# Performance work log

Measured on AMD Instinct MI355X. Metric: run time of the kernel, lower is better.

## Reference

```python
import jax, jax.numpy as jnp
import numpy as np

B, C_IN, C_OUT, H, W = 64, 1024, 1024, 16, 16
HEADS, C_RED = 8, 512  # reduced_ch = 1024 // 2
N = H * W
EPS = 1e-5  # BatchNorm eps (eval mode, running stats)
NEG_SLOPE = 0.2  # PyG GATConv default leaky_relu slope


def build_grid_edge_index(P, Pw):
    # 4-neighbor grid + one self-loop per node, directed [2, E]
    edges = []
    for i in range(P):
        for j in range(Pw):
            u = i * Pw + j
            if i - 1 >= 0: edges.append([u, u - Pw])
            if i + 1 < P:  edges.append([u, u + Pw])
            if j - 1 >= 0: edges.append([u, u - 1])
            if j + 1 < Pw: edges.append([u, u + 1])
            edges.append([u, u])
    return jnp.asarray(np.array(edges, dtype=np.int32).T)


def setup_inputs() -> dict:
    key = jax.random.key(0)
    ks = jax.random.split(key, 10)
    x = jax.random.normal(ks[0], (B, C_IN, H, W), jnp.float32)
    w_reduce = jax.random.normal(ks[1], (C_RED, C_IN), jnp.float32) * 0.02
    g_red = jnp.ones((C_RED,), jnp.float32); b_red = jnp.zeros((C_RED,), jnp.float32)
    m_red = jax.random.normal(ks[2], (C_RED,), jnp.float32) * 0.1
    v_red = jax.random.uniform(ks[3], (C_RED,), jnp.float32) + 0.5
    w_gat = jax.random.normal(ks[4], (C_RED, HEADS * C_RED), jnp.float32) * 0.02
    att_src = jax.random.normal(ks[5], (HEADS, C_RED), jnp.float32) * 0.1
    att_dst = jax.random.normal(ks[6], (HEADS, C_RED), jnp.float32) * 0.1
    gat_bias = jnp.zeros((C_RED,), jnp.float32)
    w_restore = jax.random.normal(ks[7], (C_OUT, C_RED), jnp.float32) * 0.02
    g_res = jnp.ones((C_OUT,), jnp.float32); b_res = jnp.zeros((C_OUT,), jnp.float32)
    m_res = jax.random.normal(ks[8], (C_OUT,), jnp.float32) * 0.1
    v_res = jax.random.uniform(ks[9], (C_OUT,), jnp.float32) + 0.5
    edge_index = build_grid_edge_index(H, W)
    return dict(x=x, w_reduce=w_reduce, g_red=g_red, b_red=b_red, m_red=m_red, v_red=v_red,
                w_gat=w_gat, att_src=att_src, att_dst=att_dst, gat_bias=gat_bias,
                w_restore=w_restore, g_res=g_res, b_res=b_res, m_res=m_res, v_res=v_res,
                edge_index=edge_index)


def _bn(x, g, b, m, v):  # channel-last, eval mode
    return (x - m) * (g * jax.lax.rsqrt(v + EPS)) + b


def reference(x, w_reduce, g_red, b_red, m_red, v_red, w_gat, att_src, att_dst,
              gat_bias, w_restore, g_res, b_res, m_res, v_res, edge_index):
    xh = jnp.transpose(x, (0, 2, 3, 1))                 # [B,H,W,C_in] NHWC
    res = xh                                            # identity residual (C_in == C_out)
    xr = jax.nn.relu(_bn(xh @ w_reduce.T, g_red, b_red, m_red, v_red))  # [B,H,W,C_red]
    nodes = xr.reshape(B, N, C_RED)                     # per-sample grid graph nodes

    # --- GATConv (heads=HEADS, concat=False), batched over B ---
    xp = (nodes @ w_gat).reshape(B, N, HEADS, C_RED)    # projected per-head features
    a_src = jnp.einsum('bnhc,hc->bnh', xp, att_src)
    a_dst = jnp.einsum('bnhc,hc->bnh', xp, att_dst)
    src, dst = edge_index[0], edge_index[1]
    logits = jax.nn.leaky_relu(a_src[:, src] + a_dst[:, dst], NEG_SLOPE)  # [B,E,HEADS]
    seg_max = jax.vmap(lambda a: jax.ops.segment_max(a, dst, num_segments=N))(logits)
    e = jnp.exp(logits - seg_max[:, dst])
    seg_sum = jax.vmap(lambda a: jax.ops.segment_sum(a, dst, num_segments=N))(e)
    alpha = e / seg_sum[:, dst]                          # softmax over incoming edges
    msg = alpha[..., None] * xp[:, src]                  # [B,E,HEADS,C_red]
    agg = jax.vmap(lambda m_: jax.ops.segment_sum(m_, dst, num_segments=N))(msg)
    gat_out = agg.mean(axis=2) + gat_bias                # concat=False -> head mean, [B,N,C_red]

    out = gat_out.reshape(B, H, W, C_RED) @ w_restore.T  # 1x1 restore conv
    out = _bn(out, g_res, b_res, m_res, v_res)
    out = jax.nn.relu(out + res)
    return jnp.transpose(out, (0, 3, 1, 2))              # [B,C_out,H,W]
```

## Files before the change

kernel.cpp:

```cpp
#include <hip/hip_runtime.h>


typedef unsigned short u16;
typedef __attribute__((ext_vector_type(4))) unsigned short u16x4;
typedef __attribute__((ext_vector_type(8))) unsigned short u16x8;
typedef __attribute__((ext_vector_type(8))) __bf16 bf16x8;
typedef __attribute__((ext_vector_type(2))) __bf16 bf16x2;
typedef __attribute__((ext_vector_type(4))) float f32x4;

#if defined(__has_builtin)
#if __has_builtin(__builtin_amdgcn_fdot2_f32_bf16)
#define HAVE_DOT2 1
#endif
#endif

#define B_    64
#define CIN   1024
#define CRED  512
#define COUT  1024
#define NPIX  256
#define HEADS 8
#define KGAT  4096
#define MTOT  16384
#define EPSB  1e-5f

__device__ __forceinline__ float b2f(u16 u) {
  union { unsigned u; float f; } c; c.u = ((unsigned)u) << 16; return c.f;
}
__device__ __forceinline__ u16 f2b(float f) {
  union { float f; unsigned u; } c; c.f = f;
  unsigned r = (c.u + 0x7FFFu + ((c.u >> 16) & 1u)) >> 16;
  return (u16)r;
}

__device__ __forceinline__ void gload_lds16(const void* g, void* lds) {
  __builtin_amdgcn_global_load_lds(
      (const __attribute__((address_space(1))) void*)g,
      (__attribute__((address_space(3))) void*)lds, 16, 0, 0);
}

union U8u {
  u16x8 v;
  bf16x2 p[4];
};

__global__ __launch_bounds__(512, 1) void gemm8p_kernel(
    const u16* __restrict__ A, const u16* __restrict__ Btp,
    const float* __restrict__ a_all, const float* __restrict__ gat_bias,
    u16* __restrict__ gat)
{
  extern __shared__ u16 lds[];
  u16* Ys  = lds;
  u16* alf = lds + 67584;

  const int tid = threadIdx.x;
  const int wave = tid >> 6, lane = tid & 63;
  const int wm = wave >> 2, wn = wave & 3;
  const int l15 = lane & 15, l4 = lane >> 4;

  int lin = blockIdx.y * 16 + blockIdx.x;
  lin = (lin & 7) * 128 + (lin >> 3);
  const int m0 = (lin >> 4) * 256;
  const int n0 = (lin & 15) * 256;
  const int img = lin >> 4;
  const int jbg = (lin & 15) * 32;
  const size_t nbase = (size_t)img * NPIX;

  int offS[2], ldsS[2];
#pragma unroll
  for (int i = 0; i < 2; ++i) {
    const int f = i * 512 + tid;
    const int r = f >> 2;
    const int kb = (f & 3) ^ ((r >> 1) & 3);
    offS[i] = r * 512 + kb * 8;
    ldsS[i] = (i * 512 + wave * 64) * 8;
  }
  const u16* gA = A + (size_t)m0 * 512;
  const u16* gB = Btp + (size_t)n0 * 512;

  auto stageA = [&](int kt) {
    const int bo = (kt & 3) * 16384;
    gload_lds16(gA + kt * 32 + offS[0], &lds[bo + ldsS[0]]);
    gload_lds16(gA + kt * 32 + offS[1], &lds[bo + ldsS[1]]);
  };
  auto stageB = [&](int kt) {
    const int bo = (kt & 3) * 16384 + 8192;
    gload_lds16(gB + kt * 32 + offS[0], &lds[bo + ldsS[0]]);
    gload_lds16(gB + kt * 32 + offS[1], &lds[bo + ldsS[1]]);
  };

  stageA(0); stageB(0); stageA(1); stageB(1);

  {
    const float* a_src = a_all;
    const float* a_dst = a_all + (size_t)MTOT * HEADS;
#pragma unroll
    for (int i = 0; i < 4; ++i) {
      const int nh = tid + i * 512;
      const int n = nh >> 3, h = nh & 7;
      const int gi = n >> 4, gj = n & 15;
      int vv[5];
      vv[0] = n;
      vv[1] = (gi > 0)  ? n - 16 : -1;
      vv[2] = (gi < 15) ? n + 16 : -1;
      vv[3] = (gj > 0)  ? n - 1  : -1;
      vv[4] = (gj < 15) ? n + 1  : -1;
      const float ad = a_dst[(nbase + n) * HEADS + h];
      float l[5]; float mx = -1e30f;
#pragma unroll
      for (int e = 0; e < 5; ++e) {
        if (vv[e] >= 0) {
          const float xx = a_src[(nbase + vv[e]) * HEADS + h] + ad;
          l[e] = xx > 0.f ? xx : 0.2f * xx;
          mx = fmaxf(mx, l[e]);
        } else l[e] = -1e30f;
      }
      float s = 0.f, ee[5];
#pragma unroll
      for (int e = 0; e < 5; ++e) {
        ee[e] = (vv[e] >= 0) ? __expf(l[e] - mx) : 0.f;
        s += ee[e];
      }
      const float inv = 0.125f / s;
#pragma unroll
      for (int e = 0; e < 5; ++e) alf[n * 40 + e * 8 + h] = f2b(ee[e] * inv);
    }
  }

  f32x4 acc[8][4];
#pragma unroll
  for (int i = 0; i < 8; ++i)
#pragma unroll
    for (int j = 0; j < 4; ++j) acc[i][j] = f32x4{0.f, 0.f, 0.f, 0.f};

  const int kq = (l4 ^ ((l15 >> 1) & 3)) * 8;
  const int aBase = (wm * 128 + l15) * 32 + kq;
  const int bBase = 8192 + (wn * 64 + l15) * 32 + kq;

  __syncthreads();

  for (int kt = 0; kt < 16; ++kt) {
    if (kt > 0) {
      if (kt == 15) { asm volatile("s_waitcnt vmcnt(0)" ::: "memory"); }
      else         { asm volatile("s_waitcnt vmcnt(4)" ::: "memory"); }
      __builtin_amdgcn_s_barrier();
    }
    const int bo = (kt & 3) * 16384;
    bf16x8 bfr[4], af0[4], af1[4];
#pragma unroll
    for (int f = 0; f < 4; ++f)
      bfr[f] = *(const bf16x8*)&lds[bo + bBase + f * 512];
#pragma unroll
    for (int f = 0; f < 4; ++f)
      af0[f] = *(const bf16x8*)&lds[bo + aBase + f * 512];
#pragma unroll
    for (int f = 0; f < 4; ++f)
      af1[f] = *(const bf16x8*)&lds[bo + aBase + (f + 4) * 512];
    if (kt < 14) { stageA(kt + 2); stageB(kt + 2); }
    __builtin_amdgcn_s_setprio(1);
#pragma unroll
    for (int fm = 0; fm < 4; ++fm)
#pragma unroll
      for (int fn = 0; fn < 4; ++fn)
        acc[fm][fn] = __builtin_amdgcn_mfma_f32_16x16x32_bf16(
            bfr[fn], af0[fm], acc[fm][fn], 0, 0, 0);
#pragma unroll
    for (int fm = 0; fm < 4; ++fm)
#pragma unroll
      for (int fn = 0; fn < 4; ++fn)
        acc[fm + 4][fn] = __builtin_amdgcn_mfma_f32_16x16x32_bf16(
            bfr[fn], af1[fm], acc[fm + 4][fn], 0, 0, 0);
    __builtin_amdgcn_s_setprio(0);
  }
  asm volatile("s_waitcnt vmcnt(0)" ::: "memory");
  __builtin_amdgcn_s_barrier();

#pragma unroll
  for (int fm = 0; fm < 8; ++fm) {
    const int nloc = wm * 128 + fm * 16 + l15;
#pragma unroll
    for (int fn = 0; fn < 4; ++fn) {
      const int cloc = wn * 64 + fn * 16 + l4 * 4;
      u16x4 ov;
#pragma unroll
      for (int r = 0; r < 4; ++r) ov[r] = f2b(acc[fm][fn][r]);
      *(u16x4*)&Ys[nloc * 264 + cloc] = ov;
    }
  }
  __syncthreads();

  const int b = tid & 7;
  const int nb8 = (tid >> 3) & 63;
  float fb[4];
#pragma unroll
  for (int k = 0; k < 4; ++k) fb[k] = gat_bias[jbg + b + 8 * k];
#pragma unroll
  for (int nn = 0; nn < 4; ++nn) {
    const int n = nb8 + nn * 64;
    const int gi = n >> 4, gj = n & 15;
    int vv[5];
    vv[0] = n;
    vv[1] = (gi > 0)  ? n - 16 : n;
    vv[2] = (gi < 15) ? n + 16 : n;
    vv[3] = (gj > 0)  ? n - 1  : n;
    vv[4] = (gj < 15) ? n + 1  : n;
    float o[4] = { fb[0], fb[1], fb[2], fb[3] };
#pragma unroll
    for (int e = 0; e < 5; ++e) {
      U8u au;
      au.v = *(const u16x8*)&alf[n * 40 + e * 8];
      const u16* yrow = &Ys[vv[e] * 264];
#if defined(HAVE_DOT2)
#pragma unroll
      for (int k = 0; k < 4; ++k) {
        U8u yu;
        yu.v = *(const u16x8*)&yrow[(b + 8 * k) * 8];
        float s = o[k];
        s = __builtin_amdgcn_fdot2_f32_bf16(yu.p[0], au.p[0], s, false);
        s = __builtin_amdgcn_fdot2_f32_bf16(yu.p[1], au.p[1], s, false);
        s = __builtin_amdgcn_fdot2_f32_bf16(yu.p[2], au.p[2], s, false);
        s = __builtin_amdgcn_fdot2_f32_bf16(yu.p[3], au.p[3], s, false);
        o[k] = s;
      }
#else
      float a8[8];
#pragma unroll
      for (int h = 0; h < 8; ++h) a8[h] = b2f(au.v[h]);
#pragma unroll
      for (int k = 0; k < 4; ++k) {
        const u16x8 yv = *(const u16x8*)&yrow[(b + 8 * k) * 8];
#pragma unroll
        for (int h = 0; h < 8; ++h) o[k] += a8[h] * b2f(yv[h]);
      }
#endif
    }
    const size_t gr = (nbase + n) * (size_t)CRED + jbg;
#pragma unroll
    for (int k = 0; k < 4; ++k) gat[gr + b + 8 * k] = f2b(o[k]);
  }
}

__global__ __launch_bounds__(256) void wgatp_kernel(
    const float* __restrict__ w_gat, u16* __restrict__ out)
{
  __shared__ float tile[64][65];
  const int cb = blockIdx.x;
  const int kb = blockIdx.y;
  const int t = threadIdx.x;
  const int jl = t & 7, h = (t >> 3) & 7, k4 = t >> 6;
#pragma unroll
  for (int i = 0; i < 16; ++i) {
    const int kl = k4 * 16 + i;
    tile[kl][jl * 8 + h] =
        w_gat[(size_t)(kb * 64 + kl) * KGAT + h * 512 + cb * 8 + jl];
  }
  __syncthreads();
#pragma unroll
  for (int i = 0; i < 4; ++i) {
    const int idx = i * 256 + t;
    const int cl = idx >> 4;
    const int kq = (idx & 15) * 4;
    u16x4 ov;
#pragma unroll
    for (int q = 0; q < 4; ++q) ov[q] = f2b(tile[kq + q][cl]);
    *(u16x4*)&out[(size_t)(cb * 64 + cl) * CRED + kb * 64 + kq] = ov;
  }
}

__global__ __launch_bounds__(256, 2) void gemm_redf_kernel(
    const float* __restrict__ x, const u16* __restrict__ Bt,
    u16* __restrict__ out16,
    const float* __restrict__ pg, const float* __restrict__ pb,
    const float* __restrict__ pm, const float* __restrict__ pv)
{
  __shared__ u16 As[64 * 32];
  __shared__ u16 Bs[128 * 32];
  const int tid = threadIdx.x;
  const int wave = tid >> 6, lane = tid & 63;
  const int gx = gridDim.x;
  const int nwg = gx * gridDim.y;
  int lin = blockIdx.y * gx + blockIdx.x;
  lin = (lin & 7) * (nwg >> 3) + (lin >> 3);
  const int m0 = (lin / gx) * 64, n0 = (lin % gx) * 128;
  const int bimg = m0 >> 8, p0 = m0 & 255;

  const float* xsrc = x + (size_t)bimg * CIN * NPIX + p0 + lane;

  int offB[2], dstB[2];
#pragma unroll
  for (int i = 0; i < 2; ++i) {
    const int f = i * 256 + tid;
    const int r = f >> 2;
    const int kb = (f & 3) ^ ((r >> 1) & 3);
    offB[i] = r * CIN + kb * 8;
    dstB[i] = (i * 256 + wave * 64) * 8;
  }
  const u16* gB = Bt + (size_t)n0 * CIN;

  const int aWr = (lane * 4 + (wave ^ ((lane >> 1) & 3))) * 8;

  f32x4 acc[2][4];
#pragma unroll
  for (int i = 0; i < 2; ++i)
#pragma unroll
    for (int j = 0; j < 4; ++j) acc[i][j] = f32x4{0.f, 0.f, 0.f, 0.f};

  const int wr = wave >> 1, wc = wave & 1;
  const int l15 = lane & 15, l4 = lane >> 4;
  const int kq = (l4 ^ ((l15 >> 1) & 3)) * 8;

  float av[8];
#pragma unroll
  for (int j = 0; j < 8; ++j) av[j] = xsrc[(wave * 8 + j) * NPIX];

  for (int kt = 0; kt < CIN; kt += 32) {
    u16x8 pvv;
#pragma unroll
    for (int j = 0; j < 8; ++j) pvv[j] = f2b(av[j]);
    *(u16x8*)&As[aWr] = pvv;
    gload_lds16(gB + kt + offB[0], &Bs[dstB[0]]);
    gload_lds16(gB + kt + offB[1], &Bs[dstB[1]]);
    __syncthreads();
    if (kt + 32 < CIN) {
#pragma unroll
      for (int j = 0; j < 8; ++j)
        av[j] = xsrc[(kt + 32 + wave * 8 + j) * NPIX];
    }
    bf16x8 af[2], bfr[4];
#pragma unroll
    for (int f = 0; f < 2; ++f)
      af[f] = *(const bf16x8*)&As[(wr * 32 + f * 16 + l15) * 32 + kq];
#pragma unroll
    for (int f = 0; f < 4; ++f)
      bfr[f] = *(const bf16x8*)&Bs[(wc * 64 + f * 16 + l15) * 32 + kq];
#pragma unroll
    for (int fm = 0; fm < 2; ++fm)
#pragma unroll
      for (int fn = 0; fn < 4; ++fn)
        acc[fm][fn] = __builtin_amdgcn_mfma_f32_16x16x32_bf16(
            af[fm], bfr[fn], acc[fm][fn], 0, 0, 0);
    __syncthreads();
  }

  const int rowb = m0 + wr * 32 + (lane >> 4) * 4;
#pragma unroll
  for (int fn = 0; fn < 4; ++fn) {
    const int col = n0 + wc * 64 + fn * 16 + l15;
    const float sc = pg[col] * rsqrtf(pv[col] + EPSB);
    const float off = pb[col] - pm[col] * sc;
#pragma unroll
    for (int fm = 0; fm < 2; ++fm) {
      const int row = rowb + fm * 16;
#pragma unroll
      for (int r = 0; r < 4; ++r) {
        const float y = fmaxf(acc[fm][fn][r] * sc + off, 0.f);
        out16[(size_t)(row + r) * CRED + col] = f2b(y);
      }
    }
  }
}

__global__ __launch_bounds__(256) void cvt_kernel(
    const float* __restrict__ src, u16* __restrict__ dst)
{
  const int i = (blockIdx.x * 256 + threadIdx.x) * 8;
  const float4 a = *(const float4*)&src[i];
  const float4 b = *(const float4*)&src[i + 4];
  u16x8 o;
  o[0] = f2b(a.x); o[1] = f2b(a.y); o[2] = f2b(a.z); o[3] = f2b(a.w);
  o[4] = f2b(b.x); o[5] = f2b(b.y); o[6] = f2b(b.z); o[7] = f2b(b.w);
  *(u16x8*)&dst[i] = o;
}

__global__ __launch_bounds__(256, 2) void gemm_res_kernel(
    const u16* __restrict__ A, const u16* __restrict__ Bt,
    float* __restrict__ out32,
    const float* __restrict__ pg, const float* __restrict__ pb,
    const float* __restrict__ pm, const float* __restrict__ pv,
    const float* __restrict__ auxf)
{
  const int K = CRED;
  const int gx = gridDim.x;
  const int nwg = gx * gridDim.y;
  int lin = blockIdx.y * gx + blockIdx.x;
  lin = (lin & 7) * (nwg >> 3) + (lin >> 3);
  const int m0 = (lin / gx) * 128, n0 = (lin % gx) * 128;

  __shared__ u16 As[128 * 32];
  __shared__ u16 Bs[128 * 32];
  const int tid = threadIdx.x;
  const int wave = tid >> 6, lane = tid & 63;

  int offS[2], dstS[2];
#pragma unroll
  for (int i = 0; i < 2; ++i) {
    const int f = i * 256 + tid;
    const int r = f >> 2;
    const int kb = (f & 3) ^ ((r >> 1) & 3);
    offS[i] = r * K + kb * 8;
    dstS[i] = (i * 256 + wave * 64) * 8;
  }
  const u16* gA = A + (size_t)m0 * K;
  const u16* gB = Bt + (size_t)n0 * K;

  f32x4 acc[4][4];
#pragma unroll
  for (int i = 0; i < 4; ++i)
#pragma unroll
    for (int j = 0; j < 4; ++j) acc[i][j] = f32x4{0.f, 0.f, 0.f, 0.f};

  const int wr = wave >> 1, wc = wave & 1;
  const int l15 = lane & 15, l4 = lane >> 4;
  const int kq = (l4 ^ ((l15 >> 1) & 3)) * 8;

  for (int kt = 0; kt < K; kt += 32) {
    gload_lds16(gA + kt + offS[0], &As[dstS[0]]);
    gload_lds16(gA + kt + offS[1], &As[dstS[1]]);
    gload_lds16(gB + kt + offS[0], &Bs[dstS[0]]);
    gload_lds16(gB + kt + offS[1], &Bs[dstS[1]]);
    __syncthreads();
    bf16x8 af[4], bfr[4];
#pragma unroll
    for (int f = 0; f < 4; ++f) {
      af[f]  = *(const bf16x8*)&As[(wr * 64 + f * 16 + l15) * 32 + kq];
      bfr[f] = *(const bf16x8*)&Bs[(wc * 64 + f * 16 + l15) * 32 + kq];
    }
#pragma unroll
    for (int fm = 0; fm < 4; ++fm)
#pragma unroll
      for (int fn = 0; fn < 4; ++fn)
        acc[fm][fn] = __builtin_amdgcn_mfma_f32_16x16x32_bf16(
            af[fm], bfr[fn], acc[fm][fn], 0, 0, 0);
    __syncthreads();
  }

  const int rowb = m0 + wr * 64 + (lane >> 4) * 4;
#pragma unroll
  for (int fn = 0; fn < 4; ++fn) {
    const int col = n0 + wc * 64 + fn * 16 + l15;
    const float sc = pg[col] * rsqrtf(pv[col] + EPSB);
    const float off = pb[col] - pm[col] * sc;
#pragma unroll
    for (int fm = 0; fm < 4; ++fm) {
      const int row = rowb + fm * 16;
      const int bimg = row >> 8, p0 = row & 255;
      const size_t oa = (size_t)bimg * (COUT * NPIX) + (size_t)col * NPIX + p0;
      const float4 rv = *(const float4*)&auxf[oa];
      float4 ov;
      ov.x = fmaxf(acc[fm][fn][0] * sc + off + rv.x, 0.f);
      ov.y = fmaxf(acc[fm][fn][1] * sc + off + rv.y, 0.f);
      ov.z = fmaxf(acc[fm][fn][2] * sc + off + rv.z, 0.f);
      ov.w = fmaxf(acc[fm][fn][3] * sc + off + rv.w, 0.f);
      *(float4*)&out32[oa] = ov;
    }
  }
}

__global__ __launch_bounds__(128) void attproj_kernel(
    const float* __restrict__ w_gat, const float* __restrict__ att_src,
    const float* __restrict__ att_dst, float* __restrict__ P)
{
  __shared__ float av[CRED];
  const int bi = blockIdx.x;
  const int sh = bi & 15, q = bi >> 4;
  const int s = sh >> 3, h = sh & 7;
  const float* att = (s == 0) ? att_src : att_dst;
  for (int t = threadIdx.x; t < CRED; t += 128) av[t] = att[h * CRED + t];
  __syncthreads();
  const int c = q * 128 + threadIdx.x;
  const float* wrow = w_gat + (size_t)c * KGAT + h * CRED;
  float acc = 0.f;
  for (int j = 0; j < CRED; j += 4) {
    const float4 w = *(const float4*)&wrow[j];
    acc += w.x * av[j] + w.y * av[j + 1] + w.z * av[j + 2] + w.w * av[j + 3];
  }
  P[(size_t)sh * CRED + c] = acc;
}

__global__ __launch_bounds__(256) void att_kernel(
    const u16* __restrict__ xr, const float* __restrict__ P,
    float* __restrict__ a_all)
{
  const int wave = threadIdx.x >> 6, lane = threadIdx.x & 63;
  const int m = blockIdx.x * 4 + wave;
  const int sh = lane & 15, q = lane >> 4;
  const u16* xp = xr + (size_t)m * CRED + q * 128;
  const float* Pp = P + (size_t)sh * CRED + q * 128;
  float s = 0.f;
#pragma unroll
  for (int c = 0; c < 128; c += 8) {
    u16x8 xv = *(const u16x8*)&xp[c];
#pragma unroll
    for (int t = 0; t < 8; ++t) s += b2f(xv[t]) * Pp[c + t];
  }
  s += __shfl_xor(s, 16);
  s += __shfl_xor(s, 32);
  if (q == 0)
    a_all[(size_t)(sh >> 3) * MTOT * HEADS + (size_t)m * HEADS + (sh & 7)] = s;
}

extern "C" void kernel_launch(void* const* d_in, const int* in_sizes, int n_in,
                              void* d_out, int out_size, void* d_ws, size_t ws_size,
                              hipStream_t stream)
{
  const float* x         = (const float*)d_in[0];
  const float* w_reduce  = (const float*)d_in[1];
  const float* g_red     = (const float*)d_in[2];
  const float* b_red     = (const float*)d_in[3];
  const float* m_red     = (const float*)d_in[4];
  const float* v_red     = (const float*)d_in[5];
  const float* w_gat     = (const float*)d_in[6];
  const float* att_src   = (const float*)d_in[7];
  const float* att_dst   = (const float*)d_in[8];
  const float* gat_bias  = (const float*)d_in[9];
  const float* w_restore = (const float*)d_in[10];
  const float* g_res     = (const float*)d_in[11];
  const float* b_res     = (const float*)d_in[12];
  const float* m_res     = (const float*)d_in[13];
  const float* v_res     = (const float*)d_in[14];

  constexpr size_t SZ_XR   = (size_t)MTOT * CRED * 2;
  constexpr size_t SZ_GAT  = SZ_XR;
  constexpr size_t SZ_WGT  = (size_t)KGAT * CRED * 2;
  constexpr size_t SZ_WRD  = (size_t)CRED * CIN * 2;
  constexpr size_t SZ_WRS  = (size_t)COUT * CRED * 2;
  constexpr size_t SZ_P    = (size_t)16 * CRED * 4;
  char* ws = (char*)d_ws;
  u16*   xr     = (u16*)ws;
  u16*   gat    = (u16*)(ws + SZ_XR);
  u16*   WgT2p  = (u16*)(ws + SZ_XR + SZ_GAT);
  u16*   wred_b = (u16*)(ws + SZ_XR + SZ_GAT + SZ_WGT);
  u16*   wres_b = (u16*)(ws + SZ_XR + SZ_GAT + SZ_WGT + SZ_WRD);
  float* P      = (float*)(ws + SZ_XR + SZ_GAT + SZ_WGT + SZ_WRD + SZ_WRS);
  float* a_all  = (float*)(ws + SZ_XR + SZ_GAT + SZ_WGT + SZ_WRD + SZ_WRS + SZ_P);
  float* outp   = (float*)d_out;

  hipFuncSetAttribute((const void*)gemm8p_kernel,
                      hipFuncAttributeMaxDynamicSharedMemorySize, 155648);

  wgatp_kernel<<<dim3(64, 8), 256, 0, stream>>>(w_gat, WgT2p);
  cvt_kernel<<<(CRED * CIN) / 2048, 256, 0, stream>>>(w_reduce, wred_b);
  cvt_kernel<<<(COUT * CRED) / 2048, 256, 0, stream>>>(w_restore, wres_b);
  gemm_redf_kernel<<<dim3(4, 256), 256, 0, stream>>>(
      x, wred_b, xr, g_red, b_red, m_red, v_red);
  attproj_kernel<<<64, 128, 0, stream>>>(w_gat, att_src, att_dst, P);
  att_kernel<<<MTOT / 4, 256, 0, stream>>>(xr, P, a_all);
  gemm8p_kernel<<<dim3(16, 64), 512, 155648, stream>>>(
      xr, WgT2p, a_all, gat_bias, gat);
  gemm_res_kernel<<<dim3(8, 128), 256, 0, stream>>>(
      gat, wres_b, outp, g_res, b_res, m_res, v_res, x);
  (void)in_sizes; (void)n_in; (void)out_size; (void)ws_size;
}
```

Before: 250.9 us.

## Replace restore GEMM with 256x256-tile multi-buffered pipelined kernel; merge weight conversions

The restore 1x1-conv GEMM moves from a 128x128 tile kernel with two barriers per K step to a 512-thread 256x256 tile kernel. It uses a 4-stage LDS ring with direct global-to-LDS loads issued two steps ahead, vmcnt-based waits, a single barrier per step and raised wave priority around the MFMAs. This hides load latency and raises operand reuse per tile, but uses much more LDS and registers (one block per CU) and leaves only 256 blocks. The two weight-conversion launches are merged into one kernel to save a launch.

```diff
diff --git a/kernel.cpp b/kernel.cpp
--- a/kernel.cpp
+++ b/kernel.cpp
@@ -240,6 +240,113 @@
   }
 }
 
+__global__ __launch_bounds__(512, 1) void gemm_res2_kernel(
+    const u16* __restrict__ A, const u16* __restrict__ Bt,
+    float* __restrict__ out32,
+    const float* __restrict__ pg, const float* __restrict__ pb,
+    const float* __restrict__ pm, const float* __restrict__ pv,
+    const float* __restrict__ auxf)
+{
+  extern __shared__ u16 lds[];
+  const int tid = threadIdx.x;
+  const int wave = tid >> 6, lane = tid & 63;
+  const int wm = wave >> 2, wn = wave & 3;
+  const int l15 = lane & 15, l4 = lane >> 4;
+
+  int lin = blockIdx.y * 4 + blockIdx.x;
+  lin = (lin & 7) * 32 + (lin >> 3);
+  const int m0 = (lin >> 2) * 256;
+  const int n0 = (lin & 3) * 256;
+
+  int offS[2], ldsS[2];
+#pragma unroll
+  for (int i = 0; i < 2; ++i) {
+    const int f = i * 512 + tid;
+    const int r = f >> 2;
+    const int kb = (f & 3) ^ ((r >> 1) & 3);
+    offS[i] = r * 512 + kb * 8;
+    ldsS[i] = (i * 512 + wave * 64) * 8;
+  }
+  const u16* gA = A + (size_t)m0 * 512;
+  const u16* gB = Bt + (size_t)n0 * 512;
+
+  auto stageA = [&](int kt) {
+    const int bo = (kt & 3) * 16384;
+    gload_lds16(gA + kt * 32 + offS[0], &lds[bo + ldsS[0]]);
+    gload_lds16(gA + kt * 32 + offS[1], &lds[bo + ldsS[1]]);
+  };
+  auto stageB = [&](int kt) {
+    const int bo = (kt & 3) * 16384 + 8192;
+    gload_lds16(gB + kt * 32 + offS[0], &lds[bo + ldsS[0]]);
+    gload_lds16(gB + kt * 32 + offS[1], &lds[bo + ldsS[1]]);
+  };
+
+  f32x4 acc[8][4];
+#pragma unroll
+  for (int i = 0; i < 8; ++i)
+#pragma unroll
+    for (int j = 0; j < 4; ++j) acc[i][j] = f32x4{0.f, 0.f, 0.f, 0.f};
+
+  const int kq = (l4 ^ ((l15 >> 1) & 3)) * 8;
+  const int aBase = (wm * 128 + l15) * 32 + kq;
+  const int bBase = 8192 + (wn * 64 + l15) * 32 + kq;
+
+  stageA(0); stageB(0); stageA(1); stageB(1);
+
+  for (int kt = 0; kt < 16; ++kt) {
+    if (kt == 15) { asm volatile("s_waitcnt vmcnt(0)" ::: "memory"); }
+    else         { asm volatile("s_waitcnt vmcnt(4)" ::: "memory"); }
+    __builtin_amdgcn_s_barrier();
+    const int bo = (kt & 3) * 16384;
+    bf16x8 bfr[4], af0[4], af1[4];
+#pragma unroll
+    for (int f = 0; f < 4; ++f)
+      bfr[f] = *(const bf16x8*)&lds[bo + bBase + f * 512];
+#pragma unroll
+    for (int f = 0; f < 4; ++f)
+      af0[f] = *(const bf16x8*)&lds[bo + aBase + f * 512];
+#pragma unroll
+    for (int f = 0; f < 4; ++f)
+      af1[f] = *(const bf16x8*)&lds[bo + aBase + (f + 4) * 512];
+    if (kt < 14) { stageA(kt + 2); stageB(kt + 2); }
+    __builtin_amdgcn_s_setprio(1);
+#pragma unroll
+    for (int fm = 0; fm < 4; ++fm)
+#pragma unroll
+      for (int fn = 0; fn < 4; ++fn)
+        acc[fm][fn] = __builtin_amdgcn_mfma_f32_16x16x32_bf16(
+            af0[fm], bfr[fn], acc[fm][fn], 0, 0, 0);
+#pragma unroll
+    for (int fm = 0; fm < 4; ++fm)
+#pragma unroll
+      for (int fn = 0; fn < 4; ++fn)
+        acc[fm + 4][fn] = __builtin_amdgcn_mfma_f32_16x16x32_bf16(
+            af1[fm], bfr[fn], acc[fm + 4][fn], 0, 0, 0);
+    __builtin_amdgcn_s_setprio(0);
+  }
+
+  const int rowb = m0 + wm * 128 + l4 * 4;
+#pragma unroll
+  for (int fn = 0; fn < 4; ++fn) {
+    const int col = n0 + wn * 64 + fn * 16 + l15;
+    const float sc = pg[col] * rsqrtf(pv[col] + EPSB);
+    const float off = pb[col] - pm[col] * sc;
+#pragma unroll
+    for (int fm = 0; fm < 8; ++fm) {
+      const int row = rowb + fm * 16;
+      const int bimg = row >> 8, p0 = row & 255;
+      const size_t oa = (size_t)bimg * (COUT * NPIX) + (size_t)col * NPIX + p0;
+      const float4 rv = *(const float4*)&auxf[oa];
+      float4 ov;
+      ov.x = fmaxf(acc[fm][fn][0] * sc + off + rv.x, 0.f);
+      ov.y = fmaxf(acc[fm][fn][1] * sc + off + rv.y, 0.f);
+      ov.z = fmaxf(acc[fm][fn][2] * sc + off + rv.z, 0.f);
+      ov.w = fmaxf(acc[fm][fn][3] * sc + off + rv.w, 0.f);
+      *(float4*)&out32[oa] = ov;
+    }
+  }
+}
+
 __global__ __launch_bounds__(256) void wgatp_kernel(
     const float* __restrict__ w_gat, u16* __restrict__ out)
 {
@@ -360,100 +467,20 @@
   }
 }
 
-__global__ __launch_bounds__(256) void cvt_kernel(
-    const float* __restrict__ src, u16* __restrict__ dst)
-{
-  const int i = (blockIdx.x * 256 + threadIdx.x) * 8;
+__global__ __launch_bounds__(256) void cvt2_kernel(
+    const float* __restrict__ s0, u16* __restrict__ d0,
+    const float* __restrict__ s1, u16* __restrict__ d1, int half)
+{
+  const int bi = blockIdx.x;
+  const float* src = (bi < half) ? s0 : s1;
+  u16* dst = (bi < half) ? d0 : d1;
+  const int i = ((bi < half ? bi : bi - half) * 256 + threadIdx.x) * 8;
   const float4 a = *(const float4*)&src[i];
   const float4 b = *(const float4*)&src[i + 4];
   u16x8 o;
   o[0] = f2b(a.x); o[1] = f2b(a.y); o[2] = f2b(a.z); o[3] = f2b(a.w);
   o[4] = f2b(b.x); o[5] = f2b(b.y); o[6] = f2b(b.z); o[7] = f2b(b.w);
   *(u16x8*)&dst[i] = o;
-}
-
-__global__ __launch_bounds__(256, 2) void gemm_res_kernel(
-    const u16* __restrict__ A, const u16* __restrict__ Bt,
-    float* __restrict__ out32,
-    const float* __restrict__ pg, const float* __restrict__ pb,
-    const float* __restrict__ pm, const float* __restrict__ pv,
-    const float* __restrict__ auxf)
-{
-  const int K = CRED;
-  const int gx = gridDim.x;
-  const int nwg = gx * gridDim.y;
-  int lin = blockIdx.y * gx + blockIdx.x;
-  lin = (lin & 7) * (nwg >> 3) + (lin >> 3);
-  const int m0 = (lin / gx) * 128, n0 = (lin % gx) * 128;
-
-  __shared__ u16 As[128 * 32];
-  __shared__ u16 Bs[128 * 32];
-  const int tid = threadIdx.x;
-  const int wave = tid >> 6, lane = tid & 63;
-
-  int offS[2], dstS[2];
-#pragma unroll
-  for (int i = 0; i < 2; ++i) {
-    const int f = i * 256 + tid;
-    const int r = f >> 2;
-    const int kb = (f & 3) ^ ((r >> 1) & 3);
-    offS[i] = r * K + kb * 8;
-    dstS[i] = (i * 256 + wave * 64) * 8;
-  }
-  const u16* gA = A + (size_t)m0 * K;
-  const u16* gB = Bt + (size_t)n0 * K;
-
-  f32x4 acc[4][4];
-#pragma unroll
-  for (int i = 0; i < 4; ++i)
-#pragma unroll
-    for (int j = 0; j < 4; ++j) acc[i][j] = f32x4{0.f, 0.f, 0.f, 0.f};
-
-  const int wr = wave >> 1, wc = wave & 1;
-  const int l15 = lane & 15, l4 = lane >> 4;
-  const int kq = (l4 ^ ((l15 >> 1) & 3)) * 8;
-
-  for (int kt = 0; kt < K; kt += 32) {
-    gload_lds16(gA + kt + offS[0], &As[dstS[0]]);
-    gload_lds16(gA + kt + offS[1], &As[dstS[1]]);
-    gload_lds16(gB + kt + offS[0], &Bs[dstS[0]]);
-    gload_lds16(gB + kt + offS[1], &Bs[dstS[1]]);
-    __syncthreads();
-    bf16x8 af[4], bfr[4];
-#pragma unroll
-    for (int f = 0; f < 4; ++f) {
-      af[f]  = *(const bf16x8*)&As[(wr * 64 + f * 16 + l15) * 32 + kq];
-      bfr[f] = *(const bf16x8*)&Bs[(wc * 64 + f * 16 + l15) * 32 + kq];
-    }
-#pragma unroll
-    for (int fm = 0; fm < 4; ++fm)
-#pragma unroll
-      for (int fn = 0; fn < 4; ++fn)
-        acc[fm][fn] = __builtin_amdgcn_mfma_f32_16x16x32_bf16(
-            af[fm], bfr[fn], acc[fm][fn], 0, 0, 0);
-    __syncthreads();
-  }
-
-  const int rowb = m0 + wr * 64 + (lane >> 4) * 4;
-#pragma unroll
-  for (int fn = 0; fn < 4; ++fn) {
-    const int col = n0 + wc * 64 + fn * 16 + l15;
-    const float sc = pg[col] * rsqrtf(pv[col] + EPSB);
-    const float off = pb[col] - pm[col] * sc;
-#pragma unroll
-    for (int fm = 0; fm < 4; ++fm) {
-      const int row = rowb + fm * 16;
-      const int bimg = row >> 8, p0 = row & 255;
-      const size_t oa = (size_t)bimg * (COUT * NPIX) + (size_t)col * NPIX + p0;
-      const float4 rv = *(const float4*)&auxf[oa];
-      float4 ov;
-      ov.x = fmaxf(acc[fm][fn][0] * sc + off + rv.x, 0.f);
-      ov.y = fmaxf(acc[fm][fn][1] * sc + off + rv.y, 0.f);
-      ov.z = fmaxf(acc[fm][fn][2] * sc + off + rv.z, 0.f);
-      ov.w = fmaxf(acc[fm][fn][3] * sc + off + rv.w, 0.f);
-      *(float4*)&out32[oa] = ov;
-    }
-  }
 }
 
 __global__ __launch_bounds__(128) void attproj_kernel(
@@ -537,17 +564,19 @@
 
   hipFuncSetAttribute((const void*)gemm8p_kernel,
                       hipFuncAttributeMaxDynamicSharedMemorySize, 155648);
+  hipFuncSetAttribute((const void*)gemm_res2_kernel,
+                      hipFuncAttributeMaxDynamicSharedMemorySize, 131072);
 
   wgatp_kernel<<<dim3(64, 8), 256, 0, stream>>>(w_gat, WgT2p);
-  cvt_kernel<<<(CRED * CIN) / 2048, 256, 0, stream>>>(w_reduce, wred_b);
-  cvt_kernel<<<(COUT * CRED) / 2048, 256, 0, stream>>>(w_restore, wres_b);
+  cvt2_kernel<<<512, 256, 0, stream>>>(
+      w_reduce, wred_b, w_restore, wres_b, 256);
   gemm_redf_kernel<<<dim3(4, 256), 256, 0, stream>>>(
       x, wred_b, xr, g_red, b_red, m_red, v_red);
   attproj_kernel<<<64, 128, 0, stream>>>(w_gat, att_src, att_dst, P);
   att_kernel<<<MTOT / 4, 256, 0, stream>>>(xr, P, a_all);
   gemm8p_kernel<<<dim3(16, 64), 512, 155648, stream>>>(
       xr, WgT2p, a_all, gat_bias, gat);
-  gemm_res_kernel<<<dim3(8, 128), 256, 0, stream>>>(
+  gemm_res2_kernel<<<dim3(4, 64), 512, 131072, stream>>>(
       gat, wres_b, outp, g_res, b_res, m_res, v_res, x);
   (void)in_sizes; (void)n_in; (void)out_size; (void)ws_size;
 }
```

New measurement: 250.4 us. Within noise of the previous version (-0.2%).
